# Kernel tuning notes

Hardware: AMD Instinct MI355X
Metric: run time of the kernel (lower is better)

The kernel has to match this reference:

```python
import jax, jax.numpy as jnp
import numpy as np

D_MODEL = 1024
N_HEADS = 16
D_K = D_MODEL // N_HEADS
MIN_F = 3
MAX_F = 10


def setup_inputs() -> dict:
    key = jax.random.key(0)
    ks = jax.random.split(key, 9)
    B, L = 4, 8192
    x = jax.random.normal(ks[0], (B, L, D_MODEL), jnp.float32)
    def w(k):
        return jax.random.normal(k, (D_MODEL, D_MODEL), jnp.float32) * 0.02
    def b(k):
        return jax.random.normal(k, (D_MODEL,), jnp.float32) * 0.02
    return {
        'x': x,
        'wq': w(ks[1]), 'bq': b(ks[2]),
        'wk': w(ks[3]), 'bk': b(ks[4]),
        'wv': w(ks[5]), 'bv': b(ks[6]),
        'wo': w(ks[7]), 'bo': b(ks[8]),
    }


def _sparsity_score(Q):
    # Q: (B, H, L, d_k)
    l2 = jnp.linalg.norm(Q, axis=-1)
    logp = jax.nn.log_softmax(Q, axis=-1)
    prob = jnp.exp(logp)
    entropy = -jnp.sum(prob * jnp.log(prob + 1e-9), axis=-1)
    var = jnp.var(Q, axis=-1, ddof=1)  # torch.var is unbiased by default
    return 0.5 * l2 + 0.3 * entropy + 0.2 * var


def reference(x, wq, bq, wk, bk, wv, bv, wo, bo):
    B, L, D = x.shape
    H, dk = N_HEADS, D_K
    # torch Linear: y = x @ W.T + b
    Q = (x @ wq.T + bq).reshape(B, L, H, dk).transpose(0, 2, 1, 3)  # (B,H,L,dk)
    K = (x @ wk.T + bk).reshape(B, L, H, dk).transpose(0, 2, 1, 3)
    V = (x @ wv.T + bv).reshape(B, L, H, dk).transpose(0, 2, 1, 3)

    q_scores = _sparsity_score(Q)  # (B,H,L)
    q_std = jnp.std(q_scores, axis=2, keepdims=True, ddof=1)
    q_mean = jnp.mean(q_scores, axis=2, keepdims=True)
    factor = jnp.clip(
        jnp.round(q_std / (q_mean + 1e-6) * MAX_F).astype(jnp.int32),
        MIN_F, MAX_F)  # (B,H,1)
    u = factor[:, 0, 0]  # per-batch k, taken from head 0 (matches torch code)

    # Fixed-size top-k of MAX_F; rows beyond u are masked to zero.
    _, top_idx = jax.lax.top_k(q_scores, MAX_F)  # (B,H,MAX_F)
    mask = (jnp.arange(MAX_F)[None, None, :] < u[:, None, None])  # (B,1->H,MAX_F)

    Q_sparse = jnp.take_along_axis(Q, top_idx[..., None], axis=2)  # (B,H,MAX_F,dk)
    scores = jnp.einsum('bhud,bhld->bhul', Q_sparse, K) / np.sqrt(dk).astype(np.float32)
    attn = jax.nn.softmax(scores, axis=-1)
    out = jnp.einsum('bhul,bhld->bhud', attn, V)  # (B,H,MAX_F,dk)
    out = out * mask[..., None].astype(out.dtype)

    # Scatter back into zeros; top-k indices are distinct per (b,h), so writing
    # masked zeros at the extra indices leaves those rows zero as in torch.
    bi = jnp.arange(B)[:, None, None]
    hi = jnp.arange(H)[None, :, None]
    full = jnp.zeros((B, H, L, dk), out.dtype).at[bi, hi, top_idx].set(out)

    merged = full.transpose(0, 2, 1, 3).reshape(B, L, D)
    return merged @ wo.T + bo
```

## Files before the change

kernel.cpp:

```cpp
#include <hip/hip_runtime.h>
#include <cmath>


typedef short     s16x8 __attribute__((ext_vector_type(8)));
typedef unsigned short u16x8 __attribute__((ext_vector_type(8)));
typedef unsigned short u16x4 __attribute__((ext_vector_type(4)));
typedef float     f32x4 __attribute__((ext_vector_type(4)));

__device__ __forceinline__ unsigned short f2bf(float f) {
    unsigned u = __float_as_uint(f);
    u += 0x7fffu + ((u >> 16) & 1u);
    return (unsigned short)(u >> 16);
}
__device__ __forceinline__ float bf2f(unsigned short s) {
    return __uint_as_float(((unsigned)s) << 16);
}

__device__ __forceinline__ void async16(const void* g, void* l) {
    __builtin_amdgcn_global_load_lds(
        (const __attribute__((address_space(1))) void*)g,
        (__attribute__((address_space(3))) void*)l, 16, 0, 0);
}

__global__ void k_conv(const float* __restrict__ x, const float* __restrict__ wq,
                       const float* __restrict__ wk, const float* __restrict__ wv,
                       unsigned short* __restrict__ xb, unsigned short* __restrict__ wb) {
    size_t i = (size_t)blockIdx.x * 256 + threadIdx.x;
    if (i < 8388608) {
        float4 v = ((const float4*)x)[i];
        ushort4 o; o.x = f2bf(v.x); o.y = f2bf(v.y); o.z = f2bf(v.z); o.w = f2bf(v.w);
        ((ushort4*)xb)[i] = o;
    } else {
        size_t j = i - 8388608;
        size_t wsel = j >> 18, rem = j & 262143;
        const float* src = wsel == 0 ? wq : (wsel == 1 ? wk : wv);
        float4 v = ((const float4*)src)[rem];
        ushort4 o; o.x = f2bf(v.x); o.y = f2bf(v.y); o.z = f2bf(v.z); o.w = f2bf(v.w);
        ((ushort4*)wb)[j] = o;
    }
}

__global__ __launch_bounds__(256, 3) void k_gemm_qkv(
    const unsigned short* __restrict__ xb, const unsigned short* __restrict__ wb,
    const float* __restrict__ bq, const float* __restrict__ bk, const float* __restrict__ bv,
    unsigned short* __restrict__ Kb, unsigned short* __restrict__ Vb,
    float* __restrict__ scores)
{
    __shared__ __align__(16) char lds[32768];
    int bid = blockIdx.x;
    int mt = bid / 24, rem = bid % 24;
    int wsel = rem >> 3, nt = rem & 7;
    const char* wg = (const char*)(wb + ((size_t)wsel << 20) + (size_t)nt * 128 * 1024);
    const char* xg = (const char*)(xb + (size_t)mt * 128 * 1024);
    const float* bias = wsel == 0 ? bq : (wsel == 1 ? bk : bv);
    int tid = threadIdx.x, wid = tid >> 6, lane = tid & 63;
    int wm = wid >> 1, wn = wid & 1;
    int ml = lane & 15, quad = lane >> 4;

    int srow = tid >> 3;
    int scol = ((tid & 7) ^ (srow & 7)) << 4;

    int qk0  = (quad ^ (ml & 7)) << 4;
    int aoff = (wm * 64 + ml) * 128;
    int boff = 16384 + (wn * 64 + ml) * 128;

    f32x4 acc[4][4] = {};

    for (int kt = 0; kt < 16; ++kt) {
#pragma unroll
        for (int p = 0; p < 4; ++p)
            async16(xg + (size_t)(p * 32 + srow) * 2048 + kt * 128 + scol,
                    lds + p * 4096 + tid * 16);
#pragma unroll
        for (int p = 0; p < 4; ++p)
            async16(wg + (size_t)(p * 32 + srow) * 2048 + kt * 128 + scol,
                    lds + 16384 + p * 4096 + tid * 16);
        asm volatile("s_waitcnt vmcnt(0)" ::: "memory");
        __builtin_amdgcn_s_barrier();
        asm volatile("" ::: "memory");
        s16x8 a[4][2], b[4][2];
#pragma unroll
        for (int i = 0; i < 4; ++i) {
            a[i][0] = *(const s16x8*)&lds[aoff + i * 2048 + qk0];
            a[i][1] = *(const s16x8*)&lds[aoff + i * 2048 + (qk0 ^ 64)];
        }
#pragma unroll
        for (int j = 0; j < 4; ++j) {
            b[j][0] = *(const s16x8*)&lds[boff + j * 2048 + qk0];
            b[j][1] = *(const s16x8*)&lds[boff + j * 2048 + (qk0 ^ 64)];
        }
#pragma unroll
        for (int kk = 0; kk < 2; ++kk)
#pragma unroll
            for (int i = 0; i < 4; ++i)
#pragma unroll
                for (int j = 0; j < 4; ++j)
                    acc[i][j] = __builtin_amdgcn_mfma_f32_16x16x32_bf16(a[i][kk], b[j][kk], acc[i][j], 0, 0, 0);
        asm volatile("" ::: "memory");
        __builtin_amdgcn_s_barrier();
        asm volatile("" ::: "memory");
    }

    float bvv[4];
#pragma unroll
    for (int j = 0; j < 4; ++j) bvv[j] = bias[nt * 128 + wn * 64 + j * 16 + ml];

    if (wsel == 0) {
        int hh = nt * 2 + wn;
#pragma unroll
        for (int i = 0; i < 4; ++i) {
#pragma unroll
            for (int r = 0; r < 4; ++r) {
                float q0 = acc[i][0][r] + bvv[0];
                float q1 = acc[i][1][r] + bvv[1];
                float q2 = acc[i][2][r] + bvv[2];
                float q3 = acc[i][3][r] + bvv[3];
                float mx = fmaxf(fmaxf(q0, q1), fmaxf(q2, q3));
                float sm = q0 + q1 + q2 + q3;
                float ss = q0 * q0 + q1 * q1 + q2 * q2 + q3 * q3;
#pragma unroll
                for (int off = 1; off < 16; off <<= 1) {
                    mx = fmaxf(mx, __shfl_xor(mx, off));
                    sm += __shfl_xor(sm, off);
                    ss += __shfl_xor(ss, off);
                }
                float e0 = expf(q0 - mx), e1 = expf(q1 - mx);
                float e2 = expf(q2 - mx), e3 = expf(q3 - mx);
                float S = e0 + e1 + e2 + e3;
#pragma unroll
                for (int off = 1; off < 16; off <<= 1) S += __shfl_xor(S, off);
                float is = 1.f / S;
                float p0 = e0 * is, p1 = e1 * is, p2 = e2 * is, p3 = e3 * is;
                float ent = -p0 * logf(p0 + 1e-9f) - p1 * logf(p1 + 1e-9f)
                            - p2 * logf(p2 + 1e-9f) - p3 * logf(p3 + 1e-9f);
                float mean = sm * (1.f / 64.f);
                float d0 = q0 - mean, d1 = q1 - mean, d2 = q2 - mean, d3 = q3 - mean;
                float var = d0 * d0 + d1 * d1 + d2 * d2 + d3 * d3;
#pragma unroll
                for (int off = 1; off < 16; off <<= 1) {
                    ent += __shfl_xor(ent, off);
                    var += __shfl_xor(var, off);
                }
                if (ml == 0) {
                    float sc = 0.5f * sqrtf(ss) + 0.3f * ent + 0.2f * (var * (1.f / 63.f));
                    int row = mt * 128 + wm * 64 + i * 16 + quad * 4 + r;
                    scores[(size_t)(((row >> 13) << 4) + hh) * 8192 + (row & 8191)] = sc;
                }
            }
        }
    } else {
        unsigned short* outp = wsel == 1 ? Kb : Vb;
#pragma unroll
        for (int i = 0; i < 4; ++i) {
            int grow0 = mt * 128 + wm * 64 + i * 16 + quad * 4;
#pragma unroll
            for (int j = 0; j < 4; ++j) {
                int gcol = nt * 128 + wn * 64 + j * 16 + ml;
#pragma unroll
                for (int r = 0; r < 4; ++r)
                    outp[(size_t)(grow0 + r) * 1024 + gcol] = f2bf(acc[i][j][r] + bvv[j]);
            }
        }
    }
}

__global__ __launch_bounds__(1024) void k_cand(const float* __restrict__ scores,
                                               int* __restrict__ cand, int* __restrict__ u)
{
    int pair = blockIdx.x; int t = threadIdx.x;
    __shared__ float  s_lds[8192];
    __shared__ double dred[1024];
    __shared__ float  wvv[16];
    __shared__ int    wii[16];
    const float* sp = scores + (size_t)pair * 8192;
    for (int i = t; i < 8192; i += 1024) s_lds[i] = sp[i];
    __syncthreads();

    if ((pair & 15) == 0) {
        double a0 = 0;
#pragma unroll
        for (int k = 0; k < 8; ++k) a0 += (double)s_lds[t + k * 1024];
        dred[t] = a0; __syncthreads();
        for (int st = 512; st > 0; st >>= 1) { if (t < st) dred[t] += dred[t + st]; __syncthreads(); }
        double mean = dred[0] / 8192.0;
        __syncthreads();
        double a1 = 0;
#pragma unroll
        for (int k = 0; k < 8; ++k) { double d = (double)s_lds[t + k * 1024] - mean; a1 += d * d; }
        dred[t] = a1; __syncthreads();
        for (int st = 512; st > 0; st >>= 1) { if (t < st) dred[t] += dred[t + st]; __syncthreads(); }
        if (t == 0) {
            double sd = sqrt(dred[0] / 8191.0);
            double ratio = sd / (mean + 1e-6) * 10.0;
            int f = (int)rint(ratio);
            f = f < 3 ? 3 : (f > 10 ? 10 : f);
            u[pair >> 4] = f;
        }
        __syncthreads();
    }

    for (int it = 0; it < 16; ++it) {
        float bv = -1e30f; int bi = 0x7fffffff;
#pragma unroll
        for (int k = 0; k < 8; ++k) {
            int i = t + k * 1024;
            float v = s_lds[i];
            if (v > bv || (v == bv && i < bi)) { bv = v; bi = i; }
        }
#pragma unroll
        for (int off = 32; off > 0; off >>= 1) {
            float ov = __shfl_down(bv, off);
            int   oi = __shfl_down(bi, off);
            if (ov > bv || (ov == bv && oi < bi)) { bv = ov; bi = oi; }
        }
        if ((t & 63) == 0) { wvv[t >> 6] = bv; wii[t >> 6] = bi; }
        __syncthreads();
        if (t == 0) {
            float fv = wvv[0]; int fi = wii[0];
            for (int k = 1; k < 16; ++k)
                if (wvv[k] > fv || (wvv[k] == fv && wii[k] < fi)) { fv = wvv[k]; fi = wii[k]; }
            cand[pair * 16 + it] = fi;
            s_lds[fi] = -1e30f;
        }
        __syncthreads();
    }
}

__global__ __launch_bounds__(256) void k_rescore(
    const int* __restrict__ cand, const float* __restrict__ x,
    const float* __restrict__ wq, const float* __restrict__ bq,
    double* __restrict__ cscore, float* __restrict__ cq)
{
    int bid = blockIdx.x;
    int pair = bid >> 4;
    int b = pair >> 4, h = pair & 15;
    int t = threadIdx.x;
    __shared__ float  xrow[1024];
    __shared__ double dred[256];
    __shared__ double qrow[64];

    int l = cand[bid];
    const float* xr = x + ((size_t)b * 8192 + l) * 1024;
    for (int i = t; i < 1024; i += 256) xrow[i] = xr[i];
    __syncthreads();

    int d = t >> 2, ks = t & 3;
    const float* wr = wq + (size_t)(h * 64 + d) * 1024 + ks * 256;
    const float* xs = xrow + ks * 256;
    double p = 0;
    for (int k = 0; k < 256; k += 4) {
        float4 w4 = *(const float4*)(wr + k);
        float4 x4 = *(const float4*)(xs + k);
        p += (double)w4.x * x4.x + (double)w4.y * x4.y +
             (double)w4.z * x4.z + (double)w4.w * x4.w;
    }
    dred[t] = p; __syncthreads();
    if ((t & 3) == 0)
        qrow[t >> 2] = dred[t] + dred[t + 1] + dred[t + 2] + dred[t + 3] + (double)bq[h * 64 + (t >> 2)];
    __syncthreads();

    if (t < 64) {
        double q = qrow[t];
        cq[(size_t)bid * 64 + t] = (float)q;
        double m = q;
#pragma unroll
        for (int off = 32; off > 0; off >>= 1) m = fmax(m, __shfl_down(m, off));
        m = __shfl(m, 0);
        double e = exp(q - m);
        double sum = q, sumsq = q * q, S = e;
#pragma unroll
        for (int off = 32; off > 0; off >>= 1) {
            sum += __shfl_down(sum, off);
            sumsq += __shfl_down(sumsq, off);
            S += __shfl_down(S, off);
        }
        sum = __shfl(sum, 0); sumsq = __shfl(sumsq, 0); S = __shfl(S, 0);
        double pp = e / S;
        double entc = -pp * log(pp + 1e-9);
        double mean = sum / 64.0;
        double dv = q - mean;
        double varc = dv * dv;
#pragma unroll
        for (int off = 32; off > 0; off >>= 1) {
            entc += __shfl_down(entc, off);
            varc += __shfl_down(varc, off);
        }
        if (t == 0)
            cscore[bid] = 0.5 * sqrt(sumsq) + 0.3 * entc + 0.2 * (varc / 63.0);
    }
}

__global__ void k_select(const int* __restrict__ cand, const double* __restrict__ cscore,
                         const float* __restrict__ cq,
                         int* __restrict__ sel, float* __restrict__ selq)
{
    int pair = blockIdx.x; int t = threadIdx.x;
    __shared__ int order[10];
    double sc = t < 16 ? cscore[pair * 16 + t] : -1.0e300;
    int    ci = t < 16 ? cand[pair * 16 + t]   : 0x7fffffff;
    for (int r = 0; r < 10; ++r) {
        double bs = sc; int bi = ci; int bc = t & 15;
#pragma unroll
        for (int off = 8; off > 0; off >>= 1) {
            double os = __shfl_xor(bs, off);
            int    oi = __shfl_xor(bi, off);
            int    oc = __shfl_xor(bc, off);
            if (os > bs || (os == bs && oi < bi)) { bs = os; bi = oi; bc = oc; }
        }
        if (t == 0) { order[r] = bc; sel[pair * 10 + r] = bi; }
        if ((t & 15) == bc && t < 16) { sc = -1.0e300; ci = 0x7fffffff; }
    }
    __syncthreads();
    for (int r = 0; r < 10; ++r)
        selq[((size_t)pair * 10 + r) * 64 + t] = cq[((size_t)pair * 16 + order[r]) * 64 + t];
}

__global__ __launch_bounds__(256) void k_attn_part(
    const unsigned short* __restrict__ Kb, const unsigned short* __restrict__ Vb,
    const float* __restrict__ selq, const int* __restrict__ u,
    float* __restrict__ part)
{
    int bid = blockIdx.x;
    int pair = bid >> 5, chunk = bid & 31;
    int b = pair >> 4, h = pair & 15;
    int uu = u[b];
    int t = threadIdx.x, wave = t >> 6, lane = t & 63;

    __shared__ float q_sh[10][64];
    __shared__ float w_sh[10][256];
    __shared__ unsigned short V_sh[256][68];
    __shared__ float mc_sh[10][2], Sc_sh[10][2];

    size_t kvbase = ((size_t)b * 8192 + (size_t)chunk * 256) * 1024 + h * 64;

    for (int i = t; i < uu * 64; i += 256)
        q_sh[i >> 6][i & 63] = selq[(size_t)pair * 640 + i] * 0.125f;

    const u16x8* kr = (const u16x8*)(Kb + kvbase + (size_t)t * 1024);
    const u16x8* vr = (const u16x8*)(Vb + kvbase + (size_t)t * 1024);
    u16x8 vreg[8];
#pragma unroll
    for (int k8 = 0; k8 < 8; ++k8) vreg[k8] = vr[k8];
#pragma unroll
    for (int k8 = 0; k8 < 8; ++k8) {
        *(u16x4*)&V_sh[t][k8 * 8]     = { vreg[k8][0], vreg[k8][1], vreg[k8][2], vreg[k8][3] };
        *(u16x4*)&V_sh[t][k8 * 8 + 4] = { vreg[k8][4], vreg[k8][5], vreg[k8][6], vreg[k8][7] };
    }
    float krow[64];
#pragma unroll
    for (int k8 = 0; k8 < 8; ++k8) {
        u16x8 kv = kr[k8];
#pragma unroll
        for (int e = 0; e < 8; ++e) krow[k8 * 8 + e] = bf2f(kv[e]);
    }
    __syncthreads();

    for (int rr = 0; rr < uu; ++rr) {
        const float4* qp = (const float4*)q_sh[rr];
        float acc = 0.f;
#pragma unroll
        for (int i4 = 0; i4 < 16; ++i4) {
            float4 q4 = qp[i4];
            acc += q4.x * krow[i4 * 4] + q4.y * krow[i4 * 4 + 1] +
                   q4.z * krow[i4 * 4 + 2] + q4.w * krow[i4 * 4 + 3];
        }
        w_sh[rr][t] = acc;
    }
    __syncthreads();

    for (int rr = wave; rr < uu; rr += 4) {
        float4 wv = *(const float4*)&w_sh[rr][lane * 4];
        float m4 = fmaxf(fmaxf(wv.x, wv.y), fmaxf(wv.z, wv.w));
#pragma unroll
        for (int off = 16; off > 0; off >>= 1) m4 = fmaxf(m4, __shfl_xor(m4, off));
        float e0 = expf(wv.x - m4), e1 = expf(wv.y - m4);
        float e2 = expf(wv.z - m4), e3 = expf(wv.w - m4);
        float s = e0 + e1 + e2 + e3;
#pragma unroll
        for (int off = 16; off > 0; off >>= 1) s += __shfl_xor(s, off);
        float4 ev = { e0, e1, e2, e3 };
        *(float4*)&w_sh[rr][lane * 4] = ev;
        if ((lane & 31) == 0) { int jh = lane >> 5; mc_sh[rr][jh] = m4; Sc_sh[rr][jh] = s; }
    }
    __syncthreads();

    int jh = t >> 7, tt = t & 127, dp = tt & 31;
    for (int rr = tt >> 5; rr < uu; rr += 4) {
        float o0 = 0.f, o1 = 0.f;
        int j0 = jh * 128;
        for (int j = j0; j < j0 + 128; j += 4) {
            float4 w4 = *(const float4*)&w_sh[rr][j];
#pragma unroll
            for (int jj = 0; jj < 4; ++jj) {
                unsigned v = *(const unsigned*)&V_sh[j + jj][dp * 2];
                float w1 = jj == 0 ? w4.x : (jj == 1 ? w4.y : (jj == 2 ? w4.z : w4.w));
                o0 += w1 * __uint_as_float(v << 16);
                o1 += w1 * __uint_as_float(v & 0xffff0000u);
            }
        }
        float* pp = part + (((size_t)pair * 10 + rr) * 64 + chunk * 2 + jh) * 66;
        float2 o2 = { o0, o1 };
        *(float2*)&pp[2 + dp * 2] = o2;
        if (dp == 0) { pp[0] = mc_sh[rr][jh]; pp[1] = Sc_sh[rr][jh]; }
    }
}

__global__ void k_bias(const float* __restrict__ bo, float* __restrict__ out) {
    size_t i = (size_t)blockIdx.x * 256 + threadIdx.x;
    int col4 = (int)(i & 255);
    ((float4*)out)[i] = ((const float4*)bo)[col4];
}

__global__ __launch_bounds__(256) void k_mergescatter(
    const float* __restrict__ part, const int* __restrict__ sel,
    const int* __restrict__ u, const float* __restrict__ wo,
    float* __restrict__ out)
{
    int idx = blockIdx.x; int pair = idx / 10; int r = idx % 10;
    int b = pair >> 4, h = pair & 15;
    if (r >= u[b]) return;
    int t = threadIdx.x;
    __shared__ float a_sh[64];
    if (t < 64) {
        const float* base = part + ((size_t)pair * 10 + r) * 64 * 66;
        float m = -1e30f;
        for (int c = 0; c < 64; ++c) m = fmaxf(m, base[c * 66]);
        float S = 0, o = 0;
        for (int c = 0; c < 64; ++c) {
            float f = expf(base[c * 66] - m);
            S += f * base[c * 66 + 1];
            o += f * base[c * 66 + 2 + t];
        }
        a_sh[t] = o / S;
    }
    __syncthreads();
    int l = sel[pair * 10 + r];
    float* orow = out + ((size_t)b * 8192 + l) * 1024;
    for (int j = t; j < 1024; j += 256) {
        const float* wr = wo + (size_t)j * 1024 + h * 64;
        float acc = 0;
#pragma unroll
        for (int d = 0; d < 64; d += 4) {
            float4 w4 = *(const float4*)(wr + d);
            acc += a_sh[d] * w4.x + a_sh[d + 1] * w4.y + a_sh[d + 2] * w4.z + a_sh[d + 3] * w4.w;
        }
        atomicAdd(orow + j, acc);
    }
}

static constexpr size_t OFF_XB    = 0;
static constexpr size_t OFF_WB    = OFF_XB + 67108864;
static constexpr size_t OFF_KB    = OFF_WB + 6291456;
static constexpr size_t OFF_VB    = OFF_KB + 67108864;
static constexpr size_t OFF_SC    = OFF_VB + 67108864;
static constexpr size_t OFF_U     = OFF_SC + 2097152;
static constexpr size_t OFF_SEL   = OFF_U + 256;
static constexpr size_t OFF_SELQ  = OFF_SEL + 4096;
static constexpr size_t OFF_PART  = OFF_SELQ + 163840;
static constexpr size_t OFF_CAND  = OFF_PART + 10813440;
static constexpr size_t OFF_CSC   = OFF_CAND + 4096;
static constexpr size_t OFF_CQ    = OFF_CSC + 8192;
static constexpr size_t WS_NEED   = OFF_CQ + 262144;

extern "C" void kernel_launch(void* const* d_in, const int* in_sizes, int n_in,
                              void* d_out, int out_size, void* d_ws, size_t ws_size,
                              hipStream_t stream)
{
    const float* x  = (const float*)d_in[0];
    const float* wq = (const float*)d_in[1];
    const float* bq = (const float*)d_in[2];
    const float* wk = (const float*)d_in[3];
    const float* bk = (const float*)d_in[4];
    const float* wv = (const float*)d_in[5];
    const float* bv = (const float*)d_in[6];
    const float* wo = (const float*)d_in[7];
    const float* bo = (const float*)d_in[8];
    float* out = (float*)d_out;

    if (ws_size < WS_NEED) return;

    char* ws = (char*)d_ws;
    unsigned short* xb = (unsigned short*)(ws + OFF_XB);
    unsigned short* wb = (unsigned short*)(ws + OFF_WB);
    unsigned short* Kb = (unsigned short*)(ws + OFF_KB);
    unsigned short* Vb = (unsigned short*)(ws + OFF_VB);
    float*  scores = (float*)(ws + OFF_SC);
    int*    u      = (int*)(ws + OFF_U);
    int*    sel    = (int*)(ws + OFF_SEL);
    float*  selq   = (float*)(ws + OFF_SELQ);
    float*  part   = (float*)(ws + OFF_PART);
    int*    cand   = (int*)(ws + OFF_CAND);
    double* cscore = (double*)(ws + OFF_CSC);
    float*  cq     = (float*)(ws + OFF_CQ);

    k_conv        <<<35840, 256,  0, stream>>>(x, wq, wk, wv, xb, wb);
    k_gemm_qkv    <<<6144,  256,  0, stream>>>(xb, wb, bq, bk, bv, Kb, Vb, scores);
    k_cand        <<<64,    1024, 0, stream>>>(scores, cand, u);
    k_rescore     <<<1024,  256,  0, stream>>>(cand, x, wq, bq, cscore, cq);
    k_select      <<<64,    64,   0, stream>>>(cand, cscore, cq, sel, selq);
    k_attn_part   <<<2048,  256,  0, stream>>>(Kb, Vb, selq, u, part);
    k_bias        <<<32768, 256,  0, stream>>>(bo, out);
    k_mergescatter<<<640,   256,  0, stream>>>(part, sel, u, wo, out);
}
```

Measured before the change: 701.8 us.

## Fuse rescore with select, fold bias init into attention, raise GEMM occupancy

Merges the per-candidate rescoring and top-k selection into one kernel with one block per (batch, head) pair, keeping candidate queries in LDS instead of round-tripping them through global buffers. The output bias initialisation moves into the attention-partial kernel, so each of its 2048 blocks writes a 4096-float4 slice of the output. The QKV GEMM launch bound goes from 3 to 5 waves per SIMD, which may force register spills. The fused rescore now runs only 64 blocks that serialise 16 fp64 dot products each, which lowers parallelism for that stage.

New measurement: 781.0 us. 1.11x slower.

```diff
diff --git a/kernel.cpp b/kernel.cpp
--- a/kernel.cpp
+++ b/kernel.cpp
@@ -40,7 +40,7 @@
     }
 }
 
-__global__ __launch_bounds__(256, 3) void k_gemm_qkv(
+__global__ __launch_bounds__(256, 5) void k_gemm_qkv(
     const unsigned short* __restrict__ xb, const unsigned short* __restrict__ wb,
     const float* __restrict__ bq, const float* __restrict__ bk, const float* __restrict__ bv,
     unsigned short* __restrict__ Kb, unsigned short* __restrict__ Vb,
@@ -226,42 +226,52 @@
     }
 }
 
-__global__ __launch_bounds__(256) void k_rescore(
+__global__ __launch_bounds__(256) void k_rescore_sel(
     const int* __restrict__ cand, const float* __restrict__ x,
     const float* __restrict__ wq, const float* __restrict__ bq,
-    double* __restrict__ cscore, float* __restrict__ cq)
+    int* __restrict__ sel, float* __restrict__ selq)
 {
-    int bid = blockIdx.x;
-    int pair = bid >> 4;
+    int pair = blockIdx.x;
     int b = pair >> 4, h = pair & 15;
     int t = threadIdx.x;
-    __shared__ float  xrow[1024];
+    __shared__ float  xrows[16][1024];
     __shared__ double dred[256];
-    __shared__ double qrow[64];
-
-    int l = cand[bid];
-    const float* xr = x + ((size_t)b * 8192 + l) * 1024;
-    for (int i = t; i < 1024; i += 256) xrow[i] = xr[i];
+    __shared__ double qall[16][64];
+    __shared__ double csc[16];
+    __shared__ int    cl[16];
+    __shared__ int    order[10];
+
+    if (t < 16) cl[t] = cand[pair * 16 + t];
+    __syncthreads();
+    for (int i = t; i < 16384; i += 256) {
+        int c = i >> 10, k = i & 1023;
+        xrows[c][k] = x[((size_t)b * 8192 + cl[c]) * 1024 + k];
+    }
     __syncthreads();
 
     int d = t >> 2, ks = t & 3;
     const float* wr = wq + (size_t)(h * 64 + d) * 1024 + ks * 256;
-    const float* xs = xrow + ks * 256;
-    double p = 0;
-    for (int k = 0; k < 256; k += 4) {
-        float4 w4 = *(const float4*)(wr + k);
-        float4 x4 = *(const float4*)(xs + k);
-        p += (double)w4.x * x4.x + (double)w4.y * x4.y +
-             (double)w4.z * x4.z + (double)w4.w * x4.w;
-    }
-    dred[t] = p; __syncthreads();
-    if ((t & 3) == 0)
-        qrow[t >> 2] = dred[t] + dred[t + 1] + dred[t + 2] + dred[t + 3] + (double)bq[h * 64 + (t >> 2)];
-    __syncthreads();
-
-    if (t < 64) {
-        double q = qrow[t];
-        cq[(size_t)bid * 64 + t] = (float)q;
+    for (int c = 0; c < 16; ++c) {
+        const float* xs = &xrows[c][ks * 256];
+        double p = 0;
+        for (int k = 0; k < 256; k += 4) {
+            float4 w4 = *(const float4*)(wr + k);
+            float4 x4 = *(const float4*)(xs + k);
+            p += (double)w4.x * x4.x + (double)w4.y * x4.y +
+                 (double)w4.z * x4.z + (double)w4.w * x4.w;
+        }
+        dred[t] = p; __syncthreads();
+        if ((t & 3) == 0)
+            qall[c][t >> 2] = dred[t] + dred[t + 1] + dred[t + 2] + dred[t + 3]
+                              + (double)bq[h * 64 + (t >> 2)];
+        __syncthreads();
+    }
+
+    int wv = t >> 6, lane = t & 63;
+#pragma unroll
+    for (int cg = 0; cg < 4; ++cg) {
+        int c = cg * 4 + wv;
+        double q = qall[c][lane];
         double m = q;
 #pragma unroll
         for (int off = 32; off > 0; off >>= 1) m = fmax(m, __shfl_down(m, off));
@@ -285,39 +295,37 @@
             entc += __shfl_down(entc, off);
             varc += __shfl_down(varc, off);
         }
-        if (t == 0)
-            cscore[bid] = 0.5 * sqrt(sumsq) + 0.3 * entc + 0.2 * (varc / 63.0);
-    }
-}
-
-__global__ void k_select(const int* __restrict__ cand, const double* __restrict__ cscore,
-                         const float* __restrict__ cq,
-                         int* __restrict__ sel, float* __restrict__ selq)
-{
-    int pair = blockIdx.x; int t = threadIdx.x;
-    __shared__ int order[10];
-    double sc = t < 16 ? cscore[pair * 16 + t] : -1.0e300;
-    int    ci = t < 16 ? cand[pair * 16 + t]   : 0x7fffffff;
-    for (int r = 0; r < 10; ++r) {
-        double bs = sc; int bi = ci; int bc = t & 15;
-#pragma unroll
-        for (int off = 8; off > 0; off >>= 1) {
-            double os = __shfl_xor(bs, off);
-            int    oi = __shfl_xor(bi, off);
-            int    oc = __shfl_xor(bc, off);
-            if (os > bs || (os == bs && oi < bi)) { bs = os; bi = oi; bc = oc; }
-        }
-        if (t == 0) { order[r] = bc; sel[pair * 10 + r] = bi; }
-        if ((t & 15) == bc && t < 16) { sc = -1.0e300; ci = 0x7fffffff; }
-    }
-    __syncthreads();
-    for (int r = 0; r < 10; ++r)
-        selq[((size_t)pair * 10 + r) * 64 + t] = cq[((size_t)pair * 16 + order[r]) * 64 + t];
+        if (lane == 0)
+            csc[c] = 0.5 * sqrt(sumsq) + 0.3 * entc + 0.2 * (varc / 63.0);
+    }
+    __syncthreads();
+
+    if (t < 64) {
+        double sc = t < 16 ? csc[t] : -1.0e300;
+        int    ci = t < 16 ? cl[t]  : 0x7fffffff;
+        for (int r = 0; r < 10; ++r) {
+            double bs = sc; int bi = ci; int bc = t & 15;
+#pragma unroll
+            for (int off = 8; off > 0; off >>= 1) {
+                double os = __shfl_xor(bs, off);
+                int    oi = __shfl_xor(bi, off);
+                int    oc = __shfl_xor(bc, off);
+                if (os > bs || (os == bs && oi < bi)) { bs = os; bi = oi; bc = oc; }
+            }
+            if (t == 0) { order[r] = bc; sel[pair * 10 + r] = bi; }
+            if ((t & 15) == bc && t < 16) { sc = -1.0e300; ci = 0x7fffffff; }
+        }
+    }
+    __syncthreads();
+    if (t < 64)
+        for (int r = 0; r < 10; ++r)
+            selq[((size_t)pair * 10 + r) * 64 + t] = (float)qall[order[r]][t];
 }
 
 __global__ __launch_bounds__(256) void k_attn_part(
     const unsigned short* __restrict__ Kb, const unsigned short* __restrict__ Vb,
     const float* __restrict__ selq, const int* __restrict__ u,
+    const float* __restrict__ bo, float* __restrict__ out,
     float* __restrict__ part)
 {
     int bid = blockIdx.x;
@@ -326,6 +334,13 @@
     int uu = u[b];
     int t = threadIdx.x, wave = t >> 6, lane = t & 63;
 
+    {
+        float4 bo4 = ((const float4*)bo)[t];
+        float4* ob = (float4*)out + (size_t)bid * 4096 + t;
+#pragma unroll
+        for (int j = 0; j < 16; ++j) ob[j * 256] = bo4;
+    }
+
     __shared__ float q_sh[10][64];
     __shared__ float w_sh[10][256];
     __shared__ unsigned short V_sh[256][68];
@@ -369,12 +384,12 @@
     __syncthreads();
 
     for (int rr = wave; rr < uu; rr += 4) {
-        float4 wv = *(const float4*)&w_sh[rr][lane * 4];
-        float m4 = fmaxf(fmaxf(wv.x, wv.y), fmaxf(wv.z, wv.w));
+        float4 wvv = *(const float4*)&w_sh[rr][lane * 4];
+        float m4 = fmaxf(fmaxf(wvv.x, wvv.y), fmaxf(wvv.z, wvv.w));
 #pragma unroll
         for (int off = 16; off > 0; off >>= 1) m4 = fmaxf(m4, __shfl_xor(m4, off));
-        float e0 = expf(wv.x - m4), e1 = expf(wv.y - m4);
-        float e2 = expf(wv.z - m4), e3 = expf(wv.w - m4);
+        float e0 = expf(wvv.x - m4), e1 = expf(wvv.y - m4);
+        float e2 = expf(wvv.z - m4), e3 = expf(wvv.w - m4);
         float s = e0 + e1 + e2 + e3;
 #pragma unroll
         for (int off = 16; off > 0; off >>= 1) s += __shfl_xor(s, off);
@@ -403,12 +418,6 @@
         *(float2*)&pp[2 + dp * 2] = o2;
         if (dp == 0) { pp[0] = mc_sh[rr][jh]; pp[1] = Sc_sh[rr][jh]; }
     }
-}
-
-__global__ void k_bias(const float* __restrict__ bo, float* __restrict__ out) {
-    size_t i = (size_t)blockIdx.x * 256 + threadIdx.x;
-    int col4 = (int)(i & 255);
-    ((float4*)out)[i] = ((const float4*)bo)[col4];
 }
 
 __global__ __launch_bounds__(256) void k_mergescatter(
@@ -458,9 +467,7 @@
 static constexpr size_t OFF_SELQ  = OFF_SEL + 4096;
 static constexpr size_t OFF_PART  = OFF_SELQ + 163840;
 static constexpr size_t OFF_CAND  = OFF_PART + 10813440;
-static constexpr size_t OFF_CSC   = OFF_CAND + 4096;
-static constexpr size_t OFF_CQ    = OFF_CSC + 8192;
-static constexpr size_t WS_NEED   = OFF_CQ + 262144;
+static constexpr size_t WS_NEED   = OFF_CAND + 4096;
 
 extern "C" void kernel_launch(void* const* d_in, const int* in_sizes, int n_in,
                               void* d_out, int out_size, void* d_ws, size_t ws_size,
@@ -490,15 +497,11 @@
     float*  selq   = (float*)(ws + OFF_SELQ);
     float*  part   = (float*)(ws + OFF_PART);
     int*    cand   = (int*)(ws + OFF_CAND);
-    double* cscore = (double*)(ws + OFF_CSC);
-    float*  cq     = (float*)(ws + OFF_CQ);
 
     k_conv        <<<35840, 256,  0, stream>>>(x, wq, wk, wv, xb, wb);
     k_gemm_qkv    <<<6144,  256,  0, stream>>>(xb, wb, bq, bk, bv, Kb, Vb, scores);
     k_cand        <<<64,    1024, 0, stream>>>(scores, cand, u);
-    k_rescore     <<<1024,  256,  0, stream>>>(cand, x, wq, bq, cscore, cq);
-    k_select      <<<64,    64,   0, stream>>>(cand, cscore, cq, sel, selq);
-    k_attn_part   <<<2048,  256,  0, stream>>>(Kb, Vb, selq, u, part);
-    k_bias        <<<32768, 256,  0, stream>>>(bo, out);
+    k_rescore_sel <<<64,    256,  0, stream>>>(cand, x, wq, bq, sel, selq);
+    k_attn_part   <<<2048,  256,  0, stream>>>(Kb, Vb, selq, u, bo, out, part);
     k_mergescatter<<<640,   256,  0, stream>>>(part, sel, u, wo, out);
 }
```
